# Kernel optimization log

Hardware: AMD Instinct MI355X
Metric: run time of the kernel (lower is better)

Reference implementation:

```python
import jax, jax.numpy as jnp
import numpy as np

U, I, J = 256, 512, 31          # nframes, n_actions, atom_max+1
E_IN, N_EMB, N_FIT = 3, 10, 32  # len(elements)+1, N_emb, N_fit
K = N_EMB // 4                  # slice size in the descriptor einsum


def setup_inputs() -> dict:
    key = jax.random.key(0)
    ks = jax.random.split(key, 12)
    s = 0.1
    return {
        "Sg": jax.random.normal(ks[0], (U, I, J, E_IN), jnp.float32),
        "R": jax.random.normal(ks[1], (U, I, J, 4), jnp.float32),
        # mlp_emb: Linear(3,10) -> ReLU -> Linear(10,10)  (weights stored [in,out])
        "W_emb1": jax.random.normal(ks[2], (E_IN, N_EMB), jnp.float32) * s,
        "b_emb1": jax.random.normal(ks[3], (N_EMB,), jnp.float32) * s,
        "W_emb2": jax.random.normal(ks[4], (N_EMB, N_EMB), jnp.float32) * s,
        "b_emb2": jax.random.normal(ks[5], (N_EMB,), jnp.float32) * s,
        # mlp_fit: Linear(20,32) -> ReLU -> Linear(32,32) -> ReLU -> Linear(32,1)
        "W_fit1": jax.random.normal(ks[6], (K * N_EMB, N_FIT), jnp.float32) * s,
        "b_fit1": jax.random.normal(ks[7], (N_FIT,), jnp.float32) * s,
        "W_fit2": jax.random.normal(ks[8], (N_FIT, N_FIT), jnp.float32) * s,
        "b_fit2": jax.random.normal(ks[9], (N_FIT,), jnp.float32) * s,
        "W_fit3": jax.random.normal(ks[10], (N_FIT, 1), jnp.float32) * s,
        "b_fit3": jax.random.normal(ks[11], (1,), jnp.float32) * s,
    }


def reference(Sg, R, W_emb1, b_emb1, W_emb2, b_emb2,
              W_fit1, b_fit1, W_fit2, b_fit2, W_fit3, b_fit3):
    # Embedding MLP on per-neighbor species/weight vectors: [u,i,j,3] -> [u,i,j,10]
    h = jnp.maximum(Sg @ W_emb1 + b_emb1, 0.0)
    Gmat = h @ W_emb2 + b_emb2
    # Descriptor: einsum('uijk,uijl,uiml,uimn->uikn') decomposed to avoid
    # materializing the full 4-way product; sums over both neighbor dims.
    T1 = jnp.einsum('uijk,uijl->uikl', Gmat[..., :K], R)   # [u,i,2,4]
    T2 = jnp.einsum('uiml,uimn->uiln', R, Gmat)            # [u,i,4,10]
    Dmat = jnp.einsum('uikl,uiln->uikn', T1, T2)           # [u,i,2,10]
    D = Dmat.reshape(U * I, K * N_EMB)
    # Fit MLP -> scalar Q per (frame, action)
    f = jnp.maximum(D @ W_fit1 + b_fit1, 0.0)
    f = jnp.maximum(f @ W_fit2 + b_fit2, 0.0)
    Q = f @ W_fit3 + b_fit3
    return Q.reshape(U, I, 1)
```

## Files before the change

kernel.cpp:

```cpp
#include <hip/hip_runtime.h>

constexpr int J_ = 31;
constexpr int UI = 131072;
constexpr size_t D_BYTES = (size_t)UI * 20 * 4;

constexpr int PPT   = 16;
constexpr int TILES = 2;
constexpr int SGB   = PPT * 93 * 4;
constexpr int SGPAD = 6144;
constexpr int NBLK1 = UI / (PPT * TILES);
constexpr int WOFF  = 2 * SGPAD / 4;

typedef __attribute__((address_space(1))) const void g1void;
typedef __attribute__((address_space(3))) void s3void;

__device__ __forceinline__ float qsum(float x) {
    int a = __builtin_amdgcn_update_dpp(0, __float_as_int(x), 0xB1, 0xF, 0xF, true);
    x += __int_as_float(a);
    int b = __builtin_amdgcn_update_dpp(0, __float_as_int(x), 0x4E, 0xF, 0xF, true);
    x += __int_as_float(b);
    return x;
}

__global__ __launch_bounds__(64) void dqn_phase1(
    const float* __restrict__ Sg, const float* __restrict__ R,
    const float* __restrict__ W1, const float* __restrict__ b1,
    const float* __restrict__ W2, const float* __restrict__ b2,
    float* __restrict__ Dws)
{
    __shared__ float4 sbuf4[(2 * SGPAD + 512) / 16];
    char*  sb  = reinterpret_cast<char*>(sbuf4);
    float* wl2 = reinterpret_cast<float*>(sbuf4) + WOFF;

    const int tid = threadIdx.x;
    const int lp  = tid >> 2;
    const int g   = tid & 3;

    for (int i = tid; i < 100; i += 64) wl2[i] = W2[i];
    if (tid < 10) wl2[100 + tid] = b2[tid];

    float w10[10], w11[10], w12[10], c1w[10];
    #pragma unroll
    for (int p = 0; p < 10; ++p) {
        w10[p] = W1[p]; w11[p] = W1[10 + p]; w12[p] = W1[20 + p]; c1w[p] = b1[p];
    }

    auto STAGE = [&](int tile, int off) {
        const char* gS = reinterpret_cast<const char*>(Sg) + (size_t)tile * SGB;
        #pragma unroll
        for (int r = 0; r < 6; ++r) {
            int byte = r * 1024 + tid * 16;
            if (byte > SGB - 16) byte = SGB - 16;
            __builtin_amdgcn_global_load_lds((g1void*)(gS + byte),
                                             (s3void*)(sb + off + r * 1024),
                                             16, 0, 0);
        }
    };

    auto LOADR = [&](int tile, float4& r0, float4& r1, float4& r2, float4& r3,
                     float4& r4, float4& r5, float4& r6, float4& r7) {
        const float4* rv = reinterpret_cast<const float4*>(
            R + (size_t)(tile * PPT + lp) * 124);
        r0 = rv[g];      r1 = rv[4 + g];  r2 = rv[8 + g];  r3 = rv[12 + g];
        r4 = rv[16 + g]; r5 = rv[20 + g]; r6 = rv[24 + g];
        int jt = 28 + g;
        r7 = rv[jt < J_ ? jt : (J_ - 1)];
    };

    auto COMPUTE = [&](int off, int tileIdx,
                       float4 r0, float4 r1, float4 r2, float4 r3,
                       float4 r4, float4 r5, float4 r6, float4 r7) {
        const float* sgL = reinterpret_cast<const float*>(sb + off) + lp * 93;

        float M0[10], M1[10], M2[10], M3[10];
        float4 Rs = {0.f, 0.f, 0.f, 0.f};
        #pragma unroll
        for (int p = 0; p < 10; ++p) { M0[p]=0.f; M1[p]=0.f; M2[p]=0.f; M3[p]=0.f; }

        auto PROC = [&](int j, const float4& r4v) {
            float s0 = sgL[j * 3 + 0];
            float s1 = sgL[j * 3 + 1];
            float s2 = sgL[j * 3 + 2];
            #pragma unroll
            for (int p = 0; p < 10; ++p) {
                float t = c1w[p] + s0 * w10[p] + s1 * w11[p] + s2 * w12[p];
                t = t > 0.f ? t : 0.f;
                M0[p] += r4v.x * t;
                M1[p] += r4v.y * t;
                M2[p] += r4v.z * t;
                M3[p] += r4v.w * t;
            }
            Rs.x += r4v.x; Rs.y += r4v.y; Rs.z += r4v.z; Rs.w += r4v.w;
        };

        PROC(g,      r0); PROC(4 + g,  r1); PROC(8 + g,  r2); PROC(12 + g, r3);
        PROC(16 + g, r4); PROC(20 + g, r5); PROC(24 + g, r6);
        {
            float m = (g < 3) ? 1.f : 0.f;
            float4 rm = {r7.x * m, r7.y * m, r7.z * m, r7.w * m};
            PROC(28 + g, rm);
        }

        #pragma unroll
        for (int p = 0; p < 10; ++p) {
            M0[p] = qsum(M0[p]); M1[p] = qsum(M1[p]);
            M2[p] = qsum(M2[p]); M3[p] = qsum(M3[p]);
        }
        Rs.x = qsum(Rs.x); Rs.y = qsum(Rs.y); Rs.z = qsum(Rs.z); Rs.w = qsum(Rs.w);

        float Mg[10];
        #pragma unroll
        for (int p = 0; p < 10; ++p)
            Mg[p] = (g == 0) ? M0[p] : (g == 1) ? M1[p] : (g == 2) ? M2[p] : M3[p];
        float Rsg = (g == 0) ? Rs.x : (g == 1) ? Rs.y : (g == 2) ? Rs.z : Rs.w;

        float T2g[10];
        #pragma unroll
        for (int n = 0; n < 10; ++n) T2g[n] = Rsg * wl2[100 + n];
        #pragma unroll
        for (int p = 0; p < 10; ++p) {
            float m = Mg[p];
            #pragma unroll
            for (int n = 0; n < 10; ++n) T2g[n] += m * wl2[p * 10 + n];
        }

        float D[20];
        #pragma unroll
        for (int k = 0; k < 2; ++k)
            #pragma unroll
            for (int n = 0; n < 10; ++n) D[k * 10 + n] = T2g[k] * T2g[n];
        #pragma unroll
        for (int t = 0; t < 20; ++t) D[t] = qsum(D[t]);

        float s0 = (g == 0) ? D[0] : (g == 1) ? D[5]  : (g == 2) ? D[10] : D[15];
        float s1 = (g == 0) ? D[1] : (g == 1) ? D[6]  : (g == 2) ? D[11] : D[16];
        float s2 = (g == 0) ? D[2] : (g == 1) ? D[7]  : (g == 2) ? D[12] : D[17];
        float s3 = (g == 0) ? D[3] : (g == 1) ? D[8]  : (g == 2) ? D[13] : D[18];
        float s4 = (g == 0) ? D[4] : (g == 1) ? D[9]  : (g == 2) ? D[14] : D[19];
        float* dw = Dws + (size_t)(g * 5) * UI + tileIdx * PPT + lp;
        dw[0 * UI] = s0; dw[1 * UI] = s1; dw[2 * UI] = s2;
        dw[3 * UI] = s3; dw[4 * UI] = s4;
    };

    const int t0 = blockIdx.x * TILES;
    float4 pA0,pA1,pA2,pA3,pA4,pA5,pA6,pA7;
    float4 pB0,pB1,pB2,pB3,pB4,pB5,pB6,pB7;

    STAGE(t0 + 0, 0);     LOADR(t0 + 0, pA0,pA1,pA2,pA3,pA4,pA5,pA6,pA7);
    STAGE(t0 + 1, SGPAD); LOADR(t0 + 1, pB0,pB1,pB2,pB3,pB4,pB5,pB6,pB7);
    asm volatile("s_waitcnt vmcnt(14)" ::: "memory");
    __builtin_amdgcn_sched_barrier(0);
    COMPUTE(0, t0 + 0, pA0,pA1,pA2,pA3,pA4,pA5,pA6,pA7);
    asm volatile("s_waitcnt vmcnt(5)" ::: "memory");
    __builtin_amdgcn_sched_barrier(0);
    COMPUTE(SGPAD, t0 + 1, pB0,pB1,pB2,pB3,pB4,pB5,pB6,pB7);
}

__global__ __launch_bounds__(256) void dqn_phase2(
    const float* __restrict__ Dws,
    const float* __restrict__ Wf1, const float* __restrict__ bf1,
    const float* __restrict__ Wf2, const float* __restrict__ bf2,
    const float* __restrict__ Wf3, const float* __restrict__ bf3,
    float* __restrict__ out)
{
    __shared__ float4 wlds4[448];
    const int tid = threadIdx.x;

    {
        if (tid < 160) wlds4[tid] = reinterpret_cast<const float4*>(Wf1)[tid];
        wlds4[160 + tid] = reinterpret_cast<const float4*>(Wf2)[tid];
        if (tid < 8)       wlds4[416 + tid]        = reinterpret_cast<const float4*>(bf1)[tid];
        else if (tid < 16) wlds4[424 + (tid - 8)]  = reinterpret_cast<const float4*>(bf2)[tid - 8];
        else if (tid < 24) wlds4[432 + (tid - 16)] = reinterpret_cast<const float4*>(Wf3)[tid - 16];
        else if (tid == 24) { reinterpret_cast<float*>(wlds4)[1760] = bf3[0]; }
    }
    __syncthreads();

    const int gt   = blockIdx.x * 256 + tid;
    const int pair = gt >> 2;
    const int g    = gt & 3;

    float D[20];
    #pragma unroll
    for (int t = 0; t < 20; ++t) D[t] = Dws[(size_t)t * UI + pair];

    const float* wl = reinterpret_cast<const float*>(wlds4);

    float F[8];
    {
        const float4* b4 = reinterpret_cast<const float4*>(wl + 1664 + g * 8);
        float4 x = b4[0], y = b4[1];
        F[0]=x.x; F[1]=x.y; F[2]=x.z; F[3]=x.w; F[4]=y.x; F[5]=y.y; F[6]=y.z; F[7]=y.w;
    }
    #pragma unroll
    for (int kk = 0; kk < 20; ++kk) {
        float d = D[kk];
        const float4* w4 = reinterpret_cast<const float4*>(wl + kk * 32 + g * 8);
        float4 wa = w4[0], wb = w4[1];
        F[0] += d * wa.x; F[1] += d * wa.y; F[2] += d * wa.z; F[3] += d * wa.w;
        F[4] += d * wb.x; F[5] += d * wb.y; F[6] += d * wb.z; F[7] += d * wb.w;
    }
    #pragma unroll
    for (int i = 0; i < 8; ++i) F[i] = F[i] > 0.f ? F[i] : 0.f;

    float P[8];
    #pragma unroll
    for (int i = 0; i < 8; ++i) P[i] = __shfl_xor(F[i], 1);
    const bool odd = (g & 1);
    float lo[16];
    #pragma unroll
    for (int i = 0; i < 8; ++i) {
        lo[i]     = odd ? P[i] : F[i];
        lo[8 + i] = odd ? F[i] : P[i];
    }
    float hi[16];
    #pragma unroll
    for (int i = 0; i < 16; ++i) hi[i] = __shfl_xor(lo[i], 2);
    const bool up = (g & 2);
    float f1a[32];
    #pragma unroll
    for (int i = 0; i < 16; ++i) {
        f1a[i]      = up ? hi[i] : lo[i];
        f1a[16 + i] = up ? lo[i] : hi[i];
    }

    float G[8];
    {
        const float4* b4 = reinterpret_cast<const float4*>(wl + 1696 + g * 8);
        float4 x = b4[0], y = b4[1];
        G[0]=x.x; G[1]=x.y; G[2]=x.z; G[3]=x.w; G[4]=y.x; G[5]=y.y; G[6]=y.z; G[7]=y.w;
    }
    #pragma unroll
    for (int kk = 0; kk < 32; ++kk) {
        float d = f1a[kk];
        const float4* w4 = reinterpret_cast<const float4*>(wl + 640 + kk * 32 + g * 8);
        float4 wa = w4[0], wb = w4[1];
        G[0] += d * wa.x; G[1] += d * wa.y; G[2] += d * wa.z; G[3] += d * wa.w;
        G[4] += d * wb.x; G[5] += d * wb.y; G[6] += d * wb.z; G[7] += d * wb.w;
    }
    #pragma unroll
    for (int i = 0; i < 8; ++i) G[i] = G[i] > 0.f ? G[i] : 0.f;

    float qp;
    {
        const float4* w4 = reinterpret_cast<const float4*>(wl + 1728 + g * 8);
        float4 wa = w4[0], wb = w4[1];
        qp = G[0]*wa.x + G[1]*wa.y + G[2]*wa.z + G[3]*wa.w
           + G[4]*wb.x + G[5]*wb.y + G[6]*wb.z + G[7]*wb.w;
    }
    qp += __shfl_xor(qp, 1);
    qp += __shfl_xor(qp, 2);
    float q = qp + wl[1760];

    if (g == 0) out[pair] = q;
}

struct Nb1 { float s0, s1, s2; float4 r; };
__device__ __forceinline__ Nb1 load_nb1(const float* __restrict__ sg,
                                        const float* __restrict__ rr, int j) {
    Nb1 d;
    d.s0 = sg[j * 3 + 0]; d.s1 = sg[j * 3 + 1]; d.s2 = sg[j * 3 + 2];
    d.r = *reinterpret_cast<const float4*>(rr + j * 4);
    return d;
}
__global__ __launch_bounds__(256, 2) void dqn_fused_fb(
    const float* __restrict__ Sg,  const float* __restrict__ R,
    const float* __restrict__ W1,  const float* __restrict__ b1,
    const float* __restrict__ W2,  const float* __restrict__ b2,
    const float* __restrict__ Wf1, const float* __restrict__ bf1,
    const float* __restrict__ Wf2, const float* __restrict__ bf2,
    const float* __restrict__ Wf3, const float* __restrict__ bf3,
    float* __restrict__ out)
{
    const int pair = blockIdx.x * 256 + threadIdx.x;
    const float* sg = Sg + (size_t)pair * (J_ * 3);
    const float* rr = R  + (size_t)pair * (J_ * 4);
    float w1[3][10], c1[10];
    #pragma unroll
    for (int k = 0; k < 3; ++k)
        #pragma unroll
        for (int p = 0; p < 10; ++p) w1[k][p] = W1[k * 10 + p];
    #pragma unroll
    for (int p = 0; p < 10; ++p) c1[p] = b1[p];
    float M[4][10]; float Rs[4] = {0.f,0.f,0.f,0.f};
    #pragma unroll
    for (int l = 0; l < 4; ++l)
        #pragma unroll
        for (int p = 0; p < 10; ++p) M[l][p] = 0.f;
    #pragma unroll 1
    for (int j = 0; j < J_; ++j) {
        Nb1 nb = load_nb1(sg, rr, j);
        float h[10];
        #pragma unroll
        for (int p = 0; p < 10; ++p) {
            float t = c1[p] + nb.s0*w1[0][p] + nb.s1*w1[1][p] + nb.s2*w1[2][p];
            h[p] = t > 0.f ? t : 0.f;
        }
        Rs[0]+=nb.r.x; Rs[1]+=nb.r.y; Rs[2]+=nb.r.z; Rs[3]+=nb.r.w;
        #pragma unroll
        for (int p = 0; p < 10; ++p) {
            M[0][p]+=nb.r.x*h[p]; M[1][p]+=nb.r.y*h[p];
            M[2][p]+=nb.r.z*h[p]; M[3][p]+=nb.r.w*h[p];
        }
    }
    float T2[4][10];
    #pragma unroll
    for (int l = 0; l < 4; ++l)
        #pragma unroll
        for (int n = 0; n < 10; ++n) T2[l][n] = Rs[l] * b2[n];
    #pragma unroll
    for (int p = 0; p < 10; ++p) {
        #pragma unroll
        for (int l = 0; l < 4; ++l) {
            float m = M[l][p];
            #pragma unroll
            for (int n = 0; n < 10; ++n) T2[l][n] += m * W2[p * 10 + n];
        }
    }
    float D[20];
    #pragma unroll
    for (int k = 0; k < 2; ++k)
        #pragma unroll
        for (int n = 0; n < 10; ++n)
            D[k*10+n] = T2[0][k]*T2[0][n] + T2[1][k]*T2[1][n]
                      + T2[2][k]*T2[2][n] + T2[3][k]*T2[3][n];
    float f1[32];
    #pragma unroll
    for (int o = 0; o < 32; ++o) f1[o] = bf1[o];
    #pragma unroll
    for (int kk = 0; kk < 20; ++kk) {
        const float4* wrow = reinterpret_cast<const float4*>(Wf1 + kk * 32);
        float d = D[kk];
        #pragma unroll
        for (int v = 0; v < 8; ++v) {
            float4 w = wrow[v];
            f1[4*v+0]+=d*w.x; f1[4*v+1]+=d*w.y; f1[4*v+2]+=d*w.z; f1[4*v+3]+=d*w.w;
        }
    }
    #pragma unroll
    for (int o = 0; o < 32; ++o) f1[o] = f1[o] > 0.f ? f1[o] : 0.f;
    float f2[32];
    #pragma unroll
    for (int o = 0; o < 32; ++o) f2[o] = bf2[o];
    #pragma unroll
    for (int kk = 0; kk < 32; ++kk) {
        const float4* wrow = reinterpret_cast<const float4*>(Wf2 + kk * 32);
        float d = f1[kk];
        #pragma unroll
        for (int v = 0; v < 8; ++v) {
            float4 w = wrow[v];
            f2[4*v+0]+=d*w.x; f2[4*v+1]+=d*w.y; f2[4*v+2]+=d*w.z; f2[4*v+3]+=d*w.w;
        }
    }
    #pragma unroll
    for (int o = 0; o < 32; ++o) f2[o] = f2[o] > 0.f ? f2[o] : 0.f;
    float q = bf3[0];
    #pragma unroll
    for (int o = 0; o < 32; o += 4) {
        float4 w = *reinterpret_cast<const float4*>(Wf3 + o);
        q += f2[o+0]*w.x + f2[o+1]*w.y + f2[o+2]*w.z + f2[o+3]*w.w;
    }
    out[pair] = q;
}

extern "C" void kernel_launch(void* const* d_in, const int* in_sizes, int n_in,
                              void* d_out, int out_size, void* d_ws, size_t ws_size,
                              hipStream_t stream) {
    const float* Sg  = (const float*)d_in[0];
    const float* R   = (const float*)d_in[1];
    const float* W1  = (const float*)d_in[2];
    const float* b1  = (const float*)d_in[3];
    const float* W2  = (const float*)d_in[4];
    const float* b2  = (const float*)d_in[5];
    const float* Wf1 = (const float*)d_in[6];
    const float* bf1 = (const float*)d_in[7];
    const float* Wf2 = (const float*)d_in[8];
    const float* bf2 = (const float*)d_in[9];
    const float* Wf3 = (const float*)d_in[10];
    const float* bf3 = (const float*)d_in[11];
    float* out = (float*)d_out;

    if (ws_size >= D_BYTES) {
        float* Dws = (float*)d_ws;
        dqn_phase1<<<dim3(NBLK1), dim3(64), 0, stream>>>(
            Sg, R, W1, b1, W2, b2, Dws);
        dqn_phase2<<<dim3((UI * 4) / 256), dim3(256), 0, stream>>>(
            Dws, Wf1, bf1, Wf2, bf2, Wf3, bf3, out);
    } else {
        dqn_fused_fb<<<dim3(UI / 256), dim3(256), 0, stream>>>(
            Sg, R, W1, b1, W2, b2, Wf1, bf1, Wf2, bf2, Wf3, bf3, out);
    }
}
```

Measured before the change: 46.45 us.

## Load Sg directly into registers and drop LDS staging and two-tile pipelining

The embedding/descriptor kernel no longer stages Sg into shared memory with global_load_lds, and no longer double-buffers two tiles per block. Each 64-thread block now handles one 16-pair tile. Each thread reads its 8×3 Sg values straight from global memory into registers, then waits once for all loads. W2 and b2 are read directly from global (uniform addresses) instead of being copied into LDS first. This removes LDS traffic, the staging overhead and LDS occupancy limits. In exchange, Sg reads become strided scalar loads with weaker coalescing, the launch doubles the number of blocks, and there is no overlap of loads with compute inside a block.

```diff
diff --git a/kernel.cpp b/kernel.cpp
--- a/kernel.cpp
+++ b/kernel.cpp
@@ -4,15 +4,8 @@
 constexpr int UI = 131072;
 constexpr size_t D_BYTES = (size_t)UI * 20 * 4;
 
-constexpr int PPT   = 16;
-constexpr int TILES = 2;
-constexpr int SGB   = PPT * 93 * 4;
-constexpr int SGPAD = 6144;
-constexpr int NBLK1 = UI / (PPT * TILES);
-constexpr int WOFF  = 2 * SGPAD / 4;
-
-typedef __attribute__((address_space(1))) const void g1void;
-typedef __attribute__((address_space(3))) void s3void;
+constexpr int PPB   = 16;
+constexpr int NBLK1 = UI / PPB;
 
 __device__ __forceinline__ float qsum(float x) {
     int a = __builtin_amdgcn_update_dpp(0, __float_as_int(x), 0xB1, 0xF, 0xF, true);
@@ -28,16 +21,10 @@
     const float* __restrict__ W2, const float* __restrict__ b2,
     float* __restrict__ Dws)
 {
-    __shared__ float4 sbuf4[(2 * SGPAD + 512) / 16];
-    char*  sb  = reinterpret_cast<char*>(sbuf4);
-    float* wl2 = reinterpret_cast<float*>(sbuf4) + WOFF;
-
-    const int tid = threadIdx.x;
-    const int lp  = tid >> 2;
-    const int g   = tid & 3;
-
-    for (int i = tid; i < 100; i += 64) wl2[i] = W2[i];
-    if (tid < 10) wl2[100 + tid] = b2[tid];
+    const int tid  = threadIdx.x;
+    const int lp   = tid >> 2;
+    const int g    = tid & 3;
+    const int pair = blockIdx.x * PPB + lp;
 
     float w10[10], w11[10], w12[10], c1w[10];
     #pragma unroll
@@ -45,115 +32,97 @@
         w10[p] = W1[p]; w11[p] = W1[10 + p]; w12[p] = W1[20 + p]; c1w[p] = b1[p];
     }
 
-    auto STAGE = [&](int tile, int off) {
-        const char* gS = reinterpret_cast<const char*>(Sg) + (size_t)tile * SGB;
-        #pragma unroll
-        for (int r = 0; r < 6; ++r) {
-            int byte = r * 1024 + tid * 16;
-            if (byte > SGB - 16) byte = SGB - 16;
-            __builtin_amdgcn_global_load_lds((g1void*)(gS + byte),
-                                             (s3void*)(sb + off + r * 1024),
-                                             16, 0, 0);
-        }
+    const float* sgp = Sg + (size_t)pair * 93 + 3 * g;
+    float sA[8][3];
+    #pragma unroll
+    for (int b = 0; b < 8; ++b) {
+        int idx = 12 * b;
+        if (b == 7 && g == 3) idx = 90 - 3 * g + 12 * 0;
+        const float* sp = (b == 7 && g == 3) ? (Sg + (size_t)pair * 93 + 90) : (sgp + idx);
+        sA[b][0] = sp[0]; sA[b][1] = sp[1]; sA[b][2] = sp[2];
+    }
+
+    const float4* rv = reinterpret_cast<const float4*>(R + (size_t)pair * 124);
+    float4 r0 = rv[g];      float4 r1 = rv[4 + g];
+    float4 r2 = rv[8 + g];  float4 r3 = rv[12 + g];
+    float4 r4 = rv[16 + g]; float4 r5 = rv[20 + g];
+    float4 r6 = rv[24 + g];
+    int jt = 28 + g;
+    float4 r7 = rv[jt < J_ ? jt : (J_ - 1)];
+
+    asm volatile("s_waitcnt vmcnt(0)" ::: "memory");
+    __builtin_amdgcn_sched_barrier(0);
+
+    float M0[10], M1[10], M2[10], M3[10];
+    float4 Rs = {0.f, 0.f, 0.f, 0.f};
+    #pragma unroll
+    for (int p = 0; p < 10; ++p) { M0[p]=0.f; M1[p]=0.f; M2[p]=0.f; M3[p]=0.f; }
+
+    auto PROC = [&](float s0, float s1, float s2, const float4& r4v) {
+        #pragma unroll
+        for (int p = 0; p < 10; ++p) {
+            float t = c1w[p] + s0 * w10[p] + s1 * w11[p] + s2 * w12[p];
+            t = t > 0.f ? t : 0.f;
+            M0[p] += r4v.x * t;
+            M1[p] += r4v.y * t;
+            M2[p] += r4v.z * t;
+            M3[p] += r4v.w * t;
+        }
+        Rs.x += r4v.x; Rs.y += r4v.y; Rs.z += r4v.z; Rs.w += r4v.w;
     };
 
-    auto LOADR = [&](int tile, float4& r0, float4& r1, float4& r2, float4& r3,
-                     float4& r4, float4& r5, float4& r6, float4& r7) {
-        const float4* rv = reinterpret_cast<const float4*>(
-            R + (size_t)(tile * PPT + lp) * 124);
-        r0 = rv[g];      r1 = rv[4 + g];  r2 = rv[8 + g];  r3 = rv[12 + g];
-        r4 = rv[16 + g]; r5 = rv[20 + g]; r6 = rv[24 + g];
-        int jt = 28 + g;
-        r7 = rv[jt < J_ ? jt : (J_ - 1)];
-    };
-
-    auto COMPUTE = [&](int off, int tileIdx,
-                       float4 r0, float4 r1, float4 r2, float4 r3,
-                       float4 r4, float4 r5, float4 r6, float4 r7) {
-        const float* sgL = reinterpret_cast<const float*>(sb + off) + lp * 93;
-
-        float M0[10], M1[10], M2[10], M3[10];
-        float4 Rs = {0.f, 0.f, 0.f, 0.f};
-        #pragma unroll
-        for (int p = 0; p < 10; ++p) { M0[p]=0.f; M1[p]=0.f; M2[p]=0.f; M3[p]=0.f; }
-
-        auto PROC = [&](int j, const float4& r4v) {
-            float s0 = sgL[j * 3 + 0];
-            float s1 = sgL[j * 3 + 1];
-            float s2 = sgL[j * 3 + 2];
-            #pragma unroll
-            for (int p = 0; p < 10; ++p) {
-                float t = c1w[p] + s0 * w10[p] + s1 * w11[p] + s2 * w12[p];
-                t = t > 0.f ? t : 0.f;
-                M0[p] += r4v.x * t;
-                M1[p] += r4v.y * t;
-                M2[p] += r4v.z * t;
-                M3[p] += r4v.w * t;
-            }
-            Rs.x += r4v.x; Rs.y += r4v.y; Rs.z += r4v.z; Rs.w += r4v.w;
-        };
-
-        PROC(g,      r0); PROC(4 + g,  r1); PROC(8 + g,  r2); PROC(12 + g, r3);
-        PROC(16 + g, r4); PROC(20 + g, r5); PROC(24 + g, r6);
-        {
-            float m = (g < 3) ? 1.f : 0.f;
-            float4 rm = {r7.x * m, r7.y * m, r7.z * m, r7.w * m};
-            PROC(28 + g, rm);
-        }
-
-        #pragma unroll
-        for (int p = 0; p < 10; ++p) {
-            M0[p] = qsum(M0[p]); M1[p] = qsum(M1[p]);
-            M2[p] = qsum(M2[p]); M3[p] = qsum(M3[p]);
-        }
-        Rs.x = qsum(Rs.x); Rs.y = qsum(Rs.y); Rs.z = qsum(Rs.z); Rs.w = qsum(Rs.w);
-
-        float Mg[10];
-        #pragma unroll
-        for (int p = 0; p < 10; ++p)
-            Mg[p] = (g == 0) ? M0[p] : (g == 1) ? M1[p] : (g == 2) ? M2[p] : M3[p];
-        float Rsg = (g == 0) ? Rs.x : (g == 1) ? Rs.y : (g == 2) ? Rs.z : Rs.w;
-
-        float T2g[10];
-        #pragma unroll
-        for (int n = 0; n < 10; ++n) T2g[n] = Rsg * wl2[100 + n];
-        #pragma unroll
-        for (int p = 0; p < 10; ++p) {
-            float m = Mg[p];
-            #pragma unroll
-            for (int n = 0; n < 10; ++n) T2g[n] += m * wl2[p * 10 + n];
-        }
-
-        float D[20];
-        #pragma unroll
-        for (int k = 0; k < 2; ++k)
-            #pragma unroll
-            for (int n = 0; n < 10; ++n) D[k * 10 + n] = T2g[k] * T2g[n];
-        #pragma unroll
-        for (int t = 0; t < 20; ++t) D[t] = qsum(D[t]);
-
-        float s0 = (g == 0) ? D[0] : (g == 1) ? D[5]  : (g == 2) ? D[10] : D[15];
-        float s1 = (g == 0) ? D[1] : (g == 1) ? D[6]  : (g == 2) ? D[11] : D[16];
-        float s2 = (g == 0) ? D[2] : (g == 1) ? D[7]  : (g == 2) ? D[12] : D[17];
-        float s3 = (g == 0) ? D[3] : (g == 1) ? D[8]  : (g == 2) ? D[13] : D[18];
-        float s4 = (g == 0) ? D[4] : (g == 1) ? D[9]  : (g == 2) ? D[14] : D[19];
-        float* dw = Dws + (size_t)(g * 5) * UI + tileIdx * PPT + lp;
-        dw[0 * UI] = s0; dw[1 * UI] = s1; dw[2 * UI] = s2;
-        dw[3 * UI] = s3; dw[4 * UI] = s4;
-    };
-
-    const int t0 = blockIdx.x * TILES;
-    float4 pA0,pA1,pA2,pA3,pA4,pA5,pA6,pA7;
-    float4 pB0,pB1,pB2,pB3,pB4,pB5,pB6,pB7;
-
-    STAGE(t0 + 0, 0);     LOADR(t0 + 0, pA0,pA1,pA2,pA3,pA4,pA5,pA6,pA7);
-    STAGE(t0 + 1, SGPAD); LOADR(t0 + 1, pB0,pB1,pB2,pB3,pB4,pB5,pB6,pB7);
-    asm volatile("s_waitcnt vmcnt(14)" ::: "memory");
-    __builtin_amdgcn_sched_barrier(0);
-    COMPUTE(0, t0 + 0, pA0,pA1,pA2,pA3,pA4,pA5,pA6,pA7);
-    asm volatile("s_waitcnt vmcnt(5)" ::: "memory");
-    __builtin_amdgcn_sched_barrier(0);
-    COMPUTE(SGPAD, t0 + 1, pB0,pB1,pB2,pB3,pB4,pB5,pB6,pB7);
+    PROC(sA[0][0], sA[0][1], sA[0][2], r0);
+    PROC(sA[1][0], sA[1][1], sA[1][2], r1);
+    PROC(sA[2][0], sA[2][1], sA[2][2], r2);
+    PROC(sA[3][0], sA[3][1], sA[3][2], r3);
+    PROC(sA[4][0], sA[4][1], sA[4][2], r4);
+    PROC(sA[5][0], sA[5][1], sA[5][2], r5);
+    PROC(sA[6][0], sA[6][1], sA[6][2], r6);
+    {
+        float m = (g < 3) ? 1.f : 0.f;
+        float4 rm = {r7.x * m, r7.y * m, r7.z * m, r7.w * m};
+        PROC(sA[7][0], sA[7][1], sA[7][2], rm);
+    }
+
+    #pragma unroll
+    for (int p = 0; p < 10; ++p) {
+        M0[p] = qsum(M0[p]); M1[p] = qsum(M1[p]);
+        M2[p] = qsum(M2[p]); M3[p] = qsum(M3[p]);
+    }
+    Rs.x = qsum(Rs.x); Rs.y = qsum(Rs.y); Rs.z = qsum(Rs.z); Rs.w = qsum(Rs.w);
+
+    float Mg[10];
+    #pragma unroll
+    for (int p = 0; p < 10; ++p)
+        Mg[p] = (g == 0) ? M0[p] : (g == 1) ? M1[p] : (g == 2) ? M2[p] : M3[p];
+    float Rsg = (g == 0) ? Rs.x : (g == 1) ? Rs.y : (g == 2) ? Rs.z : Rs.w;
+
+    float T2g[10];
+    #pragma unroll
+    for (int n = 0; n < 10; ++n) T2g[n] = Rsg * b2[n];
+    #pragma unroll
+    for (int p = 0; p < 10; ++p) {
+        float m = Mg[p];
+        #pragma unroll
+        for (int n = 0; n < 10; ++n) T2g[n] += m * W2[p * 10 + n];
+    }
+
+    float D[20];
+    #pragma unroll
+    for (int k = 0; k < 2; ++k)
+        #pragma unroll
+        for (int n = 0; n < 10; ++n) D[k * 10 + n] = T2g[k] * T2g[n];
+    #pragma unroll
+    for (int t = 0; t < 20; ++t) D[t] = qsum(D[t]);
+
+    float s0 = (g == 0) ? D[0] : (g == 1) ? D[5]  : (g == 2) ? D[10] : D[15];
+    float s1 = (g == 0) ? D[1] : (g == 1) ? D[6]  : (g == 2) ? D[11] : D[16];
+    float s2 = (g == 0) ? D[2] : (g == 1) ? D[7]  : (g == 2) ? D[12] : D[17];
+    float s3 = (g == 0) ? D[3] : (g == 1) ? D[8]  : (g == 2) ? D[13] : D[18];
+    float s4 = (g == 0) ? D[4] : (g == 1) ? D[9]  : (g == 2) ? D[14] : D[19];
+    float* dw = Dws + (size_t)(g * 5) * UI + pair;
+    dw[0 * UI] = s0; dw[1 * UI] = s1; dw[2 * UI] = s2;
+    dw[3 * UI] = s3; dw[4 * UI] = s4;
 }
 
 __global__ __launch_bounds__(256) void dqn_phase2(
```

Measured after the change: 42.94 us. -7.6%, faster.
